# Kernel tuning notes

Measured on AMD Instinct MI355X. Metric: run time of the kernel, lower is better.

## Reference

```python
import jax, jax.numpy as jnp
import numpy as np

B, S, E, H, D = 4, 2048, 1024, 8, 128
EPS = 1e-5


def _ln(x, g, b):
    m = jnp.mean(x, axis=-1, keepdims=True)
    v = jnp.mean((x - m) ** 2, axis=-1, keepdims=True)
    return (x - m) * jax.lax.rsqrt(v + EPS) * g + b


def _xavier(k, shape, fan_in, fan_out):
    lim = float(np.sqrt(6.0 / (fan_in + fan_out)))
    return jax.random.uniform(k, shape, jnp.float32, -lim, lim)


def setup_inputs() -> dict:
    key = jax.random.key(0)
    ks = jax.random.split(key, 10)
    return {
        "x": jax.random.normal(ks[0], (B, S, E), jnp.float32),
        # embedding_to_z: Linear(E, H*D); stored as [E, H*D] for x @ W
        "W_ez": _xavier(ks[1], (E, H * D), E, H * D),
        "b_ez": jnp.zeros((H * D,), jnp.float32),
        "U_h": _xavier(ks[2], (H, D, D), D, D),
        "U_z": _xavier(ks[3], (H, D, D), D, D),
        "b_u": jnp.zeros((H, D), jnp.float32),
        "out_shaper": _xavier(ks[4], (H, D, D), D, D),
        # shared per-step state LayerNorm
        "lns_g": jnp.ones((D,), jnp.float32),
        "lns_b": jnp.zeros((D,), jnp.float32),
        # per-head FFN: LayerNorm(D) -> Linear(D,D) -> GELU -> Linear(D,E)
        "ff_ln_g": jnp.ones((H, D), jnp.float32),
        "ff_ln_b": jnp.zeros((H, D), jnp.float32),
        "ff_W1": _xavier(ks[5], (H, D, D), D, D),
        "ff_b1": jnp.zeros((H, D), jnp.float32),
        "ff_W2": _xavier(ks[6], (H, D, E), D, E),
        "ff_b2": jnp.zeros((H, E), jnp.float32),
        # layer_attention_weights: Linear(E, 1)
        "w_att": _xavier(ks[7], (E,), E, 1),
        "b_att": jnp.zeros((), jnp.float32),
        # output LayerNorm
        "lno_g": jnp.ones((E,), jnp.float32),
        "lno_b": jnp.zeros((E,), jnp.float32),
    }


def reference(x, W_ez, b_ez, U_h, U_z, b_u, out_shaper, lns_g, lns_b,
              ff_ln_g, ff_ln_b, ff_W1, ff_b1, ff_W2, ff_b2,
              w_att, b_att, lno_g, lno_b):
    b, s, _ = x.shape
    h, d = U_h.shape[0], U_h.shape[1]
    # z tokens: [B,S,H,D]
    z = jnp.tanh((x @ W_ez + b_ez).reshape(b, s, h, d))
    # torch.einsum('bhd,hdd->bhd') takes the DIAGONAL of the second operand
    uh_diag = jnp.einsum('hii->hi', U_h)          # [H,D]
    uz_diag = jnp.einsum('hii->hi', U_z)          # [H,D]
    os_diag = jnp.einsum('hii->hi', out_shaper)   # [H,D]

    def step(h_prev, z_t):
        # h_prev, z_t: [B,H,D]
        u = jax.nn.sigmoid(h_prev * uh_diag + z_t * uz_diag + b_u)
        h_new = u * h_prev + (1.0 - u) * z_t
        h_new = _ln(h_new, lns_g, lns_b)
        return h_new, h_new

    h0 = jnp.zeros((b, h, d), x.dtype)
    _, states = jax.lax.scan(step, h0, jnp.swapaxes(z, 0, 1))  # [S,B,H,D]
    states = jnp.swapaxes(states, 0, 1)                         # [B,S,H,D]

    shaped = states * os_diag                                   # diag einsum
    hln = _ln(shaped, ff_ln_g, ff_ln_b)                         # per-head LN
    h1 = jax.nn.gelu(jnp.einsum('bshd,hde->bshe', hln, ff_W1) + ff_b1,
                     approximate=False)                         # [B,S,H,D]
    ff_out = jnp.einsum('bshd,hde->bshe', h1, ff_W2) + ff_b2    # [B,S,H,E]

    scores = jax.nn.softmax(jnp.einsum('bshe,e->bsh', ff_out, w_att) + b_att,
                            axis=2)                             # over heads
    weighted = jnp.einsum('bshe,bsh->bse', ff_out, scores)      # [B,S,E]
    return _ln(weighted, lno_g, lno_b)
```

## Files before the change

kernel.cpp:

```cpp
#include <hip/hip_runtime.h>
#include <hip/hip_bf16.h>
#include <math.h>

#define BB 4
#define SS 2048
#define EE 1024
#define HH 8
#define DD 128
#define BSR (BB*SS)
#define HD  (HH*DD)
#define LNEPS 1e-5f
#define LOG2E 1.4426950408889634f

#define NCHUNK 16
#define CHS    128
#define TPC    64
#define NTICK  (NCHUNK*TPC)
#define NWORKER 256
#define SLOTF  (BB*CHS*1024)

#define FSCAN 16
#define FB    32
#define FD    96
#define FE    160

typedef __attribute__((ext_vector_type(8))) short bf16x8;
typedef __attribute__((ext_vector_type(4))) float f32x4;

__device__ __forceinline__ ushort f2bf(float f) {
    union { float f; unsigned u; } c{f};
    unsigned r = c.u + 0x7fff + ((c.u >> 16) & 1);
    return (ushort)(r >> 16);
}
__device__ __forceinline__ float bf2f(ushort b) {
    union { unsigned u; float f; } c{(unsigned)b << 16};
    return c.f;
}

typedef __attribute__((address_space(1))) const unsigned int GUI;
typedef __attribute__((address_space(3))) unsigned int LUI;
__device__ __forceinline__ void gl_lds16(const ushort* g, ushort* l) {
    __builtin_amdgcn_global_load_lds((GUI*)g, (LUI*)l, 16, 0, 0);
}

__device__ __forceinline__ float dpp_add(float x, const int ctrl) {
    int y;
    switch (ctrl) {
        case 0x111: y = __builtin_amdgcn_update_dpp(0, __float_as_int(x), 0x111, 0xf, 0xf, true); break;
        case 0x112: y = __builtin_amdgcn_update_dpp(0, __float_as_int(x), 0x112, 0xf, 0xf, true); break;
        case 0x114: y = __builtin_amdgcn_update_dpp(0, __float_as_int(x), 0x114, 0xf, 0xf, true); break;
        case 0x118: y = __builtin_amdgcn_update_dpp(0, __float_as_int(x), 0x118, 0xf, 0xf, true); break;
        case 0x142: y = __builtin_amdgcn_update_dpp(0, __float_as_int(x), 0x142, 0xf, 0xf, true); break;
        default:    y = __builtin_amdgcn_update_dpp(0, __float_as_int(x), 0x143, 0xf, 0xf, true); break;
    }
    return x + __int_as_float(y);
}

__device__ __forceinline__ float wave_sum64(float x) {
    x = dpp_add(x, 0x111);
    x = dpp_add(x, 0x112);
    x = dpp_add(x, 0x114);
    x = dpp_add(x, 0x118);
    x = dpp_add(x, 0x142);
    x = dpp_add(x, 0x143);
    return __int_as_float(__builtin_amdgcn_readlane(__float_as_int(x), 63));
}

__device__ __forceinline__ unsigned flag_peek(unsigned* f) {
    return __hip_atomic_fetch_add(f, 0u, __ATOMIC_RELAXED, __HIP_MEMORY_SCOPE_AGENT);
}
__device__ __forceinline__ void wait_ge(unsigned* f, unsigned tgt) {
    if (threadIdx.x == 0) {
        while (flag_peek(f) < tgt) __builtin_amdgcn_s_sleep(16);
        __builtin_amdgcn_fence(__ATOMIC_ACQUIRE, "agent");
    }
    __syncthreads();
}
__device__ __forceinline__ void done_inc(unsigned* f) {
    __syncthreads();
    if (threadIdx.x == 0) {
        __builtin_amdgcn_fence(__ATOMIC_RELEASE, "agent");
        __hip_atomic_fetch_add(f, 1u, __ATOMIC_RELAXED, __HIP_MEMORY_SCOPE_AGENT);
    }
}
__device__ __forceinline__ unsigned done_inc_ret(unsigned* f, unsigned* sh) {
    __syncthreads();
    if (threadIdx.x == 0) {
        __builtin_amdgcn_fence(__ATOMIC_RELEASE, "agent");
        *sh = __hip_atomic_fetch_add(f, 1u, __ATOMIC_RELAXED, __HIP_MEMORY_SCOPE_AGENT);
    }
    __syncthreads();
    return *sh;
}

__global__ __launch_bounds__(256)
void convx2_k(const float* __restrict__ x,
              ushort* __restrict__ hi, ushort* __restrict__ lo)
{
    const size_t idx = ((size_t)blockIdx.x * 256 + threadIdx.x) * 4;
    const float4 v = *(const float4*)(x + idx);
    ushort4 oh, ol;
    oh.x = f2bf(v.x); ol.x = f2bf(v.x - bf2f(oh.x));
    oh.y = f2bf(v.y); ol.y = f2bf(v.y - bf2f(oh.y));
    oh.z = f2bf(v.z); ol.z = f2bf(v.z - bf2f(oh.z));
    oh.w = f2bf(v.w); ol.w = f2bf(v.w - bf2f(oh.w));
    *(ushort4*)(hi + idx) = oh;
    *(ushort4*)(lo + idx) = ol;
}

__global__ __launch_bounds__(256)
void prepall_k(const float* __restrict__ W_ez,
               ushort* __restrict__ Wth, ushort* __restrict__ Wtl,
               const float* __restrict__ W2, ushort* __restrict__ W2t,
               const float* __restrict__ W1, ushort* __restrict__ W1t,
               const float* __restrict__ w_att, const float* __restrict__ b2,
               const float* __restrict__ b_att,
               const float* __restrict__ Uh, const float* __restrict__ Uz,
               const float* __restrict__ Os,
               float* __restrict__ q, float* __restrict__ c,
               float* __restrict__ uh_d, float* __restrict__ uz_d,
               float* __restrict__ os_d, unsigned* __restrict__ flags)
{
    __shared__ float tile[32][33];
    const int blk = blockIdx.x;
    if (blk == 2434) {
        flags[threadIdx.x] = 0;
        return;
    }
    const int tx = threadIdx.x & 31, ty = threadIdx.x >> 5;
    if (blk < 1024) {
        const int k0 = (blk >> 5) * 32, n0 = (blk & 31) * 32;
        #pragma unroll
        for (int i = 0; i < 4; ++i)
            tile[ty + i*8][tx] = W_ez[(size_t)(k0 + ty + i*8) * 1024 + n0 + tx];
        __syncthreads();
        #pragma unroll
        for (int i = 0; i < 4; ++i) {
            const float v = tile[tx][ty + i*8];
            const ushort h = f2bf(v);
            Wth[(size_t)(n0 + ty + i*8) * 1024 + k0 + tx] = h;
            Wtl[(size_t)(n0 + ty + i*8) * 1024 + k0 + tx] = f2bf(v - bf2f(h));
        }
    } else if (blk < 2048) {
        const int b2i = blk - 1024;
        const int k0 = (b2i >> 5) * 32, n0 = (b2i & 31) * 32;
        #pragma unroll
        for (int i = 0; i < 4; ++i)
            tile[ty + i*8][tx] = W2[(size_t)(k0 + ty + i*8) * 1024 + n0 + tx];
        __syncthreads();
        #pragma unroll
        for (int i = 0; i < 4; ++i)
            W2t[(size_t)(n0 + ty + i*8) * 1024 + k0 + tx] = f2bf(tile[tx][ty + i*8]);
    } else if (blk < 2176) {
        const int idx = blk - 2048;
        const int hh = idx >> 4;
        const int k0 = (idx & 3) * 32, n0 = ((idx >> 2) & 3) * 32;
        const float* Wb = W1 + (size_t)hh * DD * DD;
        ushort*      Wtb = W1t + (size_t)hh * DD * DD;
        #pragma unroll
        for (int i = 0; i < 4; ++i)
            tile[ty + i*8][tx] = Wb[(size_t)(k0 + ty + i*8) * DD + n0 + tx];
        __syncthreads();
        #pragma unroll
        for (int i = 0; i < 4; ++i)
            Wtb[(size_t)(n0 + ty + i*8) * DD + k0 + tx] = f2bf(tile[tx][ty + i*8]);
    } else {
        const int gid  = (blk - 2176) * 256 + threadIdx.x;
        const int wave = gid >> 6, lane = gid & 63;
        if (wave < HD) {
            const float* wp = W2 + (size_t)wave * EE;
            float p = 0.f;
            for (int e = lane; e < EE; e += 64) p = fmaf(wp[e], w_att[e], p);
            #pragma unroll
            for (int off = 32; off > 0; off >>= 1) p += __shfl_xor(p, off, 64);
            if (lane == 0) {
                q[wave] = p;
                const int h = wave >> 7, d = wave & 127;
                uh_d[wave] = Uh[(size_t)h*DD*DD + (size_t)d*DD + d];
                uz_d[wave] = Uz[(size_t)h*DD*DD + (size_t)d*DD + d];
                os_d[wave] = Os[(size_t)h*DD*DD + (size_t)d*DD + d];
            }
        } else if (wave < HD + HH) {
            const int h = wave - HD;
            const float* bp = b2 + (size_t)h * EE;
            float p = 0.f;
            for (int e = lane; e < EE; e += 64) p = fmaf(bp[e], w_att[e], p);
            #pragma unroll
            for (int off = 32; off > 0; off >>= 1) p += __shfl_xor(p, off, 64);
            if (lane == 0) c[h] = p + b_att[0];
        }
    }
}

__global__ __launch_bounds__(256)
void gemm_mfma_hp(const ushort* __restrict__ Ah, const ushort* __restrict__ Al,
                  const ushort* __restrict__ Bh, const ushort* __restrict__ Bl,
                  float* __restrict__ C, const float* __restrict__ bias)
{
    __shared__ ushort AsmH[128*32], AsmL[128*32];
    __shared__ ushort BsmH[128*32], BsmL[128*32];
    const int t = threadIdx.x, lane = t & 63, w = t >> 6;
    const int wr = w >> 1, wc = w & 1;
    const int row0 = blockIdx.x * 128, col0 = blockIdx.y * 128;

    const int lr = lane >> 2;
    const int lc = (lane & 3) ^ (lr & 3);
    const size_t aoff0 = (size_t)(row0 +      w*16 + lr) * 1024 + lc*8;
    const size_t aoff1 = (size_t)(row0 + 64 + w*16 + lr) * 1024 + lc*8;
    const size_t boff0 = (size_t)(col0 +      w*16 + lr) * 1024 + lc*8;
    const size_t boff1 = (size_t)(col0 + 64 + w*16 + lr) * 1024 + lc*8;
    ushort* AH0 = AsmH + (     w*16) * 32;  ushort* AH1 = AsmH + (64 + w*16) * 32;
    ushort* AL0 = AsmL + (     w*16) * 32;  ushort* AL1 = AsmL + (64 + w*16) * 32;
    ushort* BH0 = BsmH + (     w*16) * 32;  ushort* BH1 = BsmH + (64 + w*16) * 32;
    ushort* BL0 = BsmL + (     w*16) * 32;  ushort* BL1 = BsmL + (64 + w*16) * 32;

    f32x4 acc[4][4];
    #pragma unroll
    for (int i = 0; i < 4; ++i)
        #pragma unroll
        for (int j = 0; j < 4; ++j) acc[i][j] = (f32x4){0.f,0.f,0.f,0.f};

    const int quad = lane >> 4;
    const int fr   = lane & 15;
    const int fchk = (quad ^ (lane & 3)) * 8;

    for (int k0 = 0; k0 < 1024; k0 += 32) {
        __syncthreads();
        gl_lds16(Ah + aoff0 + k0, AH0);
        gl_lds16(Ah + aoff1 + k0, AH1);
        gl_lds16(Bh + boff0 + k0, BH0);
        gl_lds16(Bh + boff1 + k0, BH1);
        gl_lds16(Al + aoff0 + k0, AL0);
        gl_lds16(Al + aoff1 + k0, AL1);
        gl_lds16(Bl + boff0 + k0, BL0);
        gl_lds16(Bl + boff1 + k0, BL1);
        __syncthreads();

        bf16x8 afh[4], afl[4], bfh[4], bfl[4];
        #pragma unroll
        for (int i = 0; i < 4; ++i) {
            const int ra = (wr*64 + i*16 + fr) * 32 + fchk;
            afh[i] = *(const bf16x8*)(AsmH + ra);
            afl[i] = *(const bf16x8*)(AsmL + ra);
            const int rb = (wc*64 + i*16 + fr) * 32 + fchk;
            bfh[i] = *(const bf16x8*)(BsmH + rb);
            bfl[i] = *(const bf16x8*)(BsmL + rb);
        }
        #pragma unroll
        for (int i = 0; i < 4; ++i)
            #pragma unroll
            for (int j = 0; j < 4; ++j) {
                acc[i][j] = __builtin_amdgcn_mfma_f32_16x16x32_bf16(
                    afh[i], bfl[j], acc[i][j], 0, 0, 0);
                acc[i][j] = __builtin_amdgcn_mfma_f32_16x16x32_bf16(
                    afl[i], bfh[j], acc[i][j], 0, 0, 0);
                acc[i][j] = __builtin_amdgcn_mfma_f32_16x16x32_bf16(
                    afh[i], bfh[j], acc[i][j], 0, 0, 0);
            }
    }

    float colv[4];
    #pragma unroll
    for (int tj = 0; tj < 4; ++tj)
        colv[tj] = bias[col0 + wc*64 + tj*16 + fr];
    #pragma unroll
    for (int ti = 0; ti < 4; ++ti)
        #pragma unroll
        for (int i = 0; i < 4; ++i) {
            const int row = row0 + wr*64 + ti*16 + quad*4 + i;
            #pragma unroll
            for (int tj = 0; tj < 4; ++tj) {
                const int col = col0 + wc*64 + tj*16 + fr;
                C[(size_t)row*1024 + col] = tanhf(acc[ti][tj][i] + colv[tj]);
            }
        }
}

__global__ __launch_bounds__(256)
void pipeline_k(const float* __restrict__ z,
                const float* __restrict__ uh_d, const float* __restrict__ uz_d,
                const float* __restrict__ b_u,
                const float* __restrict__ lns_g, const float* __restrict__ lns_b,
                ushort* __restrict__ stb,
                const float* __restrict__ os_d,
                const float* __restrict__ ffg, const float* __restrict__ ffb,
                const ushort* __restrict__ W1t, const float* __restrict__ ff_b1,
                const float* __restrict__ qv, const float* __restrict__ cv,
                ushort* __restrict__ h1b, float* __restrict__ logits,
                const ushort* __restrict__ W2t, const float* __restrict__ ff_b2,
                float* __restrict__ wslots,
                const float* __restrict__ lno_g, const float* __restrict__ lno_b,
                float* __restrict__ out,
                unsigned* __restrict__ flags)
{
    if (blockIdx.x < 32) {
        if (threadIdx.x >= 64) return;
        const int bh = blockIdx.x;
        const int b = bh >> 3, h = bh & 7;
        const int l = threadIdx.x;
        const int d0 = 2*l, d1 = d0 + 1;

        const float uhn0 = -uh_d[h*DD+d0] * LOG2E, uhn1 = -uh_d[h*DD+d1] * LOG2E;
        const float uzn0 = -uz_d[h*DD+d0] * LOG2E, uzn1 = -uz_d[h*DD+d1] * LOG2E;
        const float bun0 = -b_u [h*DD+d0] * LOG2E, bun1 = -b_u [h*DD+d1] * LOG2E;
        const float g0  = lns_g[d0], g1 = lns_g[d1];
        const float be0 = lns_b[d0], be1 = lns_b[d1];
        const float A0 = g0 * uhn0, A1 = g1 * uhn1;
        const float bunB0 = fmaf(be0, uhn0, bun0);
        const float bunB1 = fmaf(be1, uhn1, bun1);

        const float* zp = z + ((size_t)b * SS * HH + h) * DD + d0;
        unsigned* op = (unsigned*)(stb + (size_t)b * SS * HD + h * DD) + l;

        const int CH = 8;
        float2 zc[CH], zn[CH];
        float pb0[CH], pb1[CH];
        #pragma unroll
        for (int i = 0; i < CH; ++i) zc[i] = *(const float2*)(zp + (size_t)i*HD);
        #pragma unroll
        for (int i = 0; i < CH; ++i) {
            pb0[i] = fmaf(zc[i].x, uzn0, bunB0);
            pb1[i] = fmaf(zc[i].y, uzn1, bunB1);
        }

        float r_c, wp0, wp1, W0, W1, dv0, dv1;

#define PACK_STORE(HP0, HP1, OFF) do {                                       \
            const unsigned pu0 = __float_as_uint(HP0) + 0x8000u;             \
            const unsigned pu1 = __float_as_uint(HP1) + 0x8000u;             \
            op[(size_t)(OFF) * (HD/2)] =                                     \
                __builtin_amdgcn_perm(pu1, pu0, 0x07060302u);                \
        } while (0)

#define SCAN_STEP(ZX, ZY, PB0v, PB1v, ZNX, ZNY, OFF) do {                    \
            const float t0 = fmaf(r_c, W0, (PB0v));                          \
            const float t1 = fmaf(r_c, W1, (PB1v));                          \
            const float e0 = __builtin_amdgcn_exp2f(t0);                     \
            const float e1 = __builtin_amdgcn_exp2f(t1);                     \
            const float u0 = __builtin_amdgcn_rcpf(1.f + e0);                \
            const float u1 = __builtin_amdgcn_rcpf(1.f + e1);                \
            const float hn0 = fmaf(u0, dv0, (ZX));                           \
            const float hn1 = fmaf(u1, dv1, (ZY));                           \
            const float s1 = wave_sum64(hn0 + hn1);                          \
            const float s2 = wave_sum64(fmaf(hn0, hn0, hn1*hn1));            \
            const float m   = s1 * (1.f/128.f);                              \
            const float var = fmaf(s2, 1.f/128.f, -m*m);                     \
            r_c = __builtin_amdgcn_rsqf(var + LNEPS);                        \
            wp0 = hn0 - m; wp1 = hn1 - m;                                    \
            W0 = wp0 * A0; W1 = wp1 * A1;                                    \
            const float hp0 = fmaf(wp0, r_c * g0, be0);                      \
            const float hp1 = fmaf(wp1, r_c * g1, be1);                      \
            PACK_STORE(hp0, hp1, OFF);                                       \
            dv0 = hp0 - (ZNX); dv1 = hp1 - (ZNY);                            \
        } while (0)

        {
            const float z0 = zc[0].x, z1 = zc[0].y;
            const float t0 = fmaf(z0, uzn0, bun0);
            const float t1 = fmaf(z1, uzn1, bun1);
            const float e0 = __builtin_amdgcn_exp2f(t0);
            const float e1 = __builtin_amdgcn_exp2f(t1);
            const float u0 = __builtin_amdgcn_rcpf(1.f + e0);
            const float u1 = __builtin_amdgcn_rcpf(1.f + e1);
            const float hn0 = fmaf(u0, -z0, z0);
            const float hn1 = fmaf(u1, -z1, z1);
            const float s1 = wave_sum64(hn0 + hn1);
            const float s2 = wave_sum64(fmaf(hn0, hn0, hn1*hn1));
            const float m   = s1 * (1.f/128.f);
            const float var = fmaf(s2, 1.f/128.f, -m*m);
            r_c = __builtin_amdgcn_rsqf(var + LNEPS);
            wp0 = hn0 - m; wp1 = hn1 - m;
            W0 = wp0 * A0; W1 = wp1 * A1;
            const float hp0 = fmaf(wp0, r_c * g0, be0);
            const float hp1 = fmaf(wp1, r_c * g1, be1);
            PACK_STORE(hp0, hp1, 0);
            dv0 = hp0 - zc[1].x; dv1 = hp1 - zc[1].y;
        }

        #pragma unroll
        for (int i = 0; i < CH; ++i)
            zn[i] = *(const float2*)(zp + (size_t)(CH+i)*HD);
        #pragma unroll
        for (int i = 1; i < CH; ++i) {
            const float znx = (i+1 < CH) ? zc[i+1].x : zn[0].x;
            const float zny = (i+1 < CH) ? zc[i+1].y : zn[0].y;
            SCAN_STEP(zc[i].x, zc[i].y, pb0[i], pb1[i], znx, zny, i);
        }
        #pragma unroll
        for (int i = 0; i < CH; ++i) {
            zc[i] = zn[i];
            pb0[i] = fmaf(zn[i].x, uzn0, bunB0);
            pb1[i] = fmaf(zn[i].y, uzn1, bunB1);
        }

        for (int s0 = CH; s0 < SS; s0 += CH) {
            if (s0 + CH < SS) {
                #pragma unroll
                for (int i = 0; i < CH; ++i)
                    zn[i] = *(const float2*)(zp + (size_t)(s0+CH+i)*HD);
            } else {
                #pragma unroll
                for (int i = 0; i < CH; ++i) zn[i] = make_float2(0.f, 0.f);
            }
            #pragma unroll
            for (int i = 0; i < CH; ++i) {
                const float znx = (i+1 < CH) ? zc[i+1].x : zn[0].x;
                const float zny = (i+1 < CH) ? zc[i+1].y : zn[0].y;
                SCAN_STEP(zc[i].x, zc[i].y, pb0[i], pb1[i], znx, zny, s0 + i);
            }
            #pragma unroll
            for (int i = 0; i < CH; ++i) {
                zc[i] = zn[i];
                pb0[i] = fmaf(zn[i].x, uzn0, bunB0);
                pb1[i] = fmaf(zn[i].y, uzn1, bunB1);
            }
            if ((s0 & (CHS-1)) == CHS - CH) {
                if (threadIdx.x == 0) {
                    __builtin_amdgcn_fence(__ATOMIC_RELEASE, "agent");
                    __hip_atomic_fetch_add(&flags[FSCAN + (s0 >> 7)], 1u,
                                           __ATOMIC_RELAXED, __HIP_MEMORY_SCOPE_AGENT);
                }
            }
        }
#undef SCAN_STEP
#undef PACK_STORE
        return;
    }

    __shared__ ushort ApS[4*128*32];
    __shared__ ushort Bsm[128*32];
    __shared__ float  sLDS[128][8];
    __shared__ float  lpart[128][2];
    __shared__ unsigned s_tk, s_old;
    const int tid = threadIdx.x;
    const int lane = tid & 63, w = tid >> 6;
    const int wr = w >> 1, wc = w & 1;
    const int lr = lane >> 2;
    const int lc = (lane & 3) ^ (lr & 3);
    const int quad = lane >> 4;
    const int fr   = lane & 15;
    const int fchk = (quad ^ (lane & 3)) * 8;

    for (;;) {
        __syncthreads();
        if (tid == 0) s_tk = __hip_atomic_fetch_add(&flags[0], 1u,
                               __ATOMIC_RELAXED, __HIP_MEMORY_SCOPE_AGENT);
        __syncthreads();
        const unsigned tk = s_tk;
        if (tk >= NTICK) return;
        const int c = (int)(tk / TPC);
        const int r = (int)(tk % TPC);

        if (r < 32) {
            wait_ge(&flags[FSCAN + c], 32);
            const int bb = r >> 3, hh = r & 7;
            const int row0 = bb*SS + c*CHS;

            {
                const int l = lane;
                const int d0 = 2*l, d1 = d0 + 1;
                const float osd0 = os_d[hh*DD + d0], osd1 = os_d[hh*DD + d1];
                const float fg0 = ffg[hh*DD + d0], fg1 = ffg[hh*DD + d1];
                const float fb0 = ffb[hh*DD + d0], fb1 = ffb[hh*DD + d1];
                const unsigned* st_u = (const unsigned*)stb;
                const int p  = l >> 4;
                const int j  = (l >> 2) & 3;
                unsigned* ApU = (unsigned*)ApS;
                for (int it = 0; it < 32; ++it) {
                    const int rloc = it*4 + w;
                    const unsigned v = st_u[(size_t)(row0 + rloc)*512 + hh*64 + l];
                    const float x0 = bf2f((ushort)(v & 0xffff)) * osd0;
                    const float x1 = bf2f((ushort)(v >> 16))    * osd1;
                    float s1 = x0 + x1;
                    float s2 = fmaf(x0, x0, x1*x1);
                    #pragma unroll
                    for (int off = 32; off > 0; off >>= 1) {
                        s1 += __shfl_xor(s1, off, 64);
                        s2 += __shfl_xor(s2, off, 64);
                    }
                    const float m   = s1 * (1.f/128.f);
                    const float var = fmaf(s2, 1.f/128.f, -m*m);
                    const float rr  = rsqrtf(var + LNEPS);
                    const float o0 = fmaf((x0 - m)*rr, fg0, fb0);
                    const float o1 = fmaf((x1 - m)*rr, fg1, fb1);
                    const unsigned pv = (unsigned)f2bf(o0) | ((unsigned)f2bf(o1) << 16);
                    const int js = j ^ (rloc & 3);
                    ApU[p*2048 + rloc*16 + js*4 + (l & 3)] = pv;
                }
            }
            __syncthreads();

            const ushort* Bg0 = W1t + (size_t)hh*DD*DD + (     w*16 + lr) * DD + lc*8;
            const ushort* Bg1 = W1t + (size_t)hh*DD*DD + (64 + w*16 + lr) * DD + lc*8;
            ushort* Bl0 = Bsm + (     w*16) * 32;
            ushort* Bl1 = Bsm + (64 + w*16) * 32;

            f32x4 acc[4][4];
            #pragma unroll
            for (int i = 0; i < 4; ++i)
                #pragma unroll
                for (int j2 = 0; j2 < 4; ++j2) acc[i][j2] = (f32x4){0.f,0.f,0.f,0.f};

            for (int k0 = 0; k0 < 128; k0 += 32) {
                __syncthreads();
                gl_lds16(Bg0 + k0, Bl0);
                gl_lds16(Bg1 + k0, Bl1);
                __syncthreads();

                const ushort* Ap = ApS + (k0 >> 5) * 4096;
                bf16x8 af[4], bf[4];
                #pragma unroll
                for (int i = 0; i < 4; ++i) {
                    af[i] = *(const bf16x8*)(Ap + (wr*64 + i*16 + fr)*32 + fchk);
                    bf[i] = *(const bf16x8*)(Bsm + (wc*64 + i*16 + fr)*32 + fchk);
                }
                #pragma unroll
                for (int i = 0; i < 4; ++i)
                    #pragma unroll
                    for (int j2 = 0; j2 < 4; ++j2)
                        acc[i][j2] = __builtin_amdgcn_mfma_f32_16x16x32_bf16(
                            af[i], bf[j2], acc[i][j2], 0, 0, 0);
            }

            float colv[4], qh[4];
            #pragma unroll
            for (int tj = 0; tj < 4; ++tj) {
                const int col = wc*64 + tj*16 + fr;
                colv[tj] = ff_b1[hh*DD + col];
                qh[tj]   = qv[hh*DD + col];
            }
            #pragma unroll
            for (int ti = 0; ti < 4; ++ti)
                #pragma unroll
                for (int i = 0; i < 4; ++i) {
                    const int row = row0 + wr*64 + ti*16 + quad*4 + i;
                    float p = 0.f;
                    #pragma unroll
                    for (int tj = 0; tj < 4; ++tj) {
                        const int col = wc*64 + tj*16 + fr;
                        float v = acc[ti][tj][i] + colv[tj];
                        v = 0.5f * v * (1.f + erff(v * 0.70710678118654752f));
                        h1b[(size_t)row*1024 + hh*DD + col] = f2bf(v);
                        p = fmaf(v, qh[tj], p);
                    }
                    p = dpp_add(p, 0x111);
                    p = dpp_add(p, 0x112);
                    p = dpp_add(p, 0x114);
                    p = dpp_add(p, 0x118);
                    if (fr == 15)
                        lpart[wr*64 + ti*16 + quad*4 + i][wc] = p;
                }
            __syncthreads();
            if (tid < 128)
                logits[(size_t)(row0 + tid)*HH + hh] = lpart[tid][0] + lpart[tid][1] + cv[hh];
            done_inc(&flags[FB + c*4 + bb]);
        } else {
            const int sub = r - 32;
            const int bb = sub >> 3, cb = sub & 7;
            wait_ge(&flags[FB + c*4 + bb], 8);
            if (c >= 8) wait_ge(&flags[FE + (c-8)*4 + bb], 1);
            const int row0 = bb*SS + c*CHS, col0 = cb*128;
            float* wslot = wslots + (size_t)(c & 7) * SLOTF;

            if (tid < 128) {
                const float4 l03 = *(const float4*)(logits + (size_t)(row0 + tid)*8);
                const float4 l47 = *(const float4*)(logits + (size_t)(row0 + tid)*8 + 4);
                float lv[8] = {l03.x,l03.y,l03.z,l03.w,l47.x,l47.y,l47.z,l47.w};
                float mx = -1e30f;
                #pragma unroll
                for (int i = 0; i < 8; ++i) mx = fmaxf(mx, lv[i]);
                float den = 0.f;
                #pragma unroll
                for (int i = 0; i < 8; ++i) den += __expf(lv[i] - mx);
                const float rden = 1.f / den;
                #pragma unroll
                for (int i = 0; i < 8; ++i) sLDS[tid][i] = __expf(lv[i] - mx) * rden;
            }
            __syncthreads();

            const ushort* Bg0 = W2t + (size_t)(col0 +      w*16 + lr) * 1024 + lc*8;
            const ushort* Bg1 = W2t + (size_t)(col0 + 64 + w*16 + lr) * 1024 + lc*8;
            ushort* Bl0 = Bsm + (     w*16) * 32;
            ushort* Bl1 = Bsm + (64 + w*16) * 32;
            const int rl0 = w*16 + lr, rl1 = 64 + w*16 + lr;

            f32x4 acc[4][4];
            #pragma unroll
            for (int i = 0; i < 4; ++i)
                #pragma unroll
                for (int j2 = 0; j2 < 4; ++j2) acc[i][j2] = (f32x4){0.f,0.f,0.f,0.f};

            for (int k0 = 0; k0 < 1024; k0 += 32) {
                __syncthreads();
                {
                    const int kk = k0 + lc*8;
                    const int hidx = kk >> 7;
                    bf16x8 a0 = *(const bf16x8*)(h1b + (size_t)(row0 + rl0)*1024 + kk);
                    bf16x8 a1 = *(const bf16x8*)(h1b + (size_t)(row0 + rl1)*1024 + kk);
                    const float sc0 = sLDS[rl0][hidx];
                    const float sc1 = sLDS[rl1][hidx];
                    bf16x8 w0, w1;
                    #pragma unroll
                    for (int e = 0; e < 8; ++e) {
                        w0[e] = (short)f2bf(bf2f((ushort)a0[e]) * sc0);
                        w1[e] = (short)f2bf(bf2f((ushort)a1[e]) * sc1);
                    }
                    *(bf16x8*)(ApS + (     w*16)*32 + lane*8) = w0;
                    *(bf16x8*)(ApS + (64 + w*16)*32 + lane*8) = w1;
                }
                gl_lds16(Bg0 + k0, Bl0);
                gl_lds16(Bg1 + k0, Bl1);
                __syncthreads();

                bf16x8 af[4], bf[4];
                #pragma unroll
                for (int i = 0; i < 4; ++i) {
                    af[i] = *(const bf16x8*)(ApS + (wr*64 + i*16 + fr)*32 + fchk);
                    bf[i] = *(const bf16x8*)(Bsm + (wc*64 + i*16 + fr)*32 + fchk);
                }
                #pragma unroll
                for (int i = 0; i < 4; ++i)
                    #pragma unroll
                    for (int j2 = 0; j2 < 4; ++j2)
                        acc[i][j2] = __builtin_amdgcn_mfma_f32_16x16x32_bf16(
                            af[i], bf[j2], acc[i][j2], 0, 0, 0);
            }

            float b2v[4][HH];
            #pragma unroll
            for (int tj = 0; tj < 4; ++tj) {
                const int col = col0 + wc*64 + tj*16 + fr;
                #pragma unroll
                for (int h = 0; h < HH; ++h) b2v[tj][h] = ff_b2[(size_t)h*EE + col];
            }
            #pragma unroll
            for (int ti = 0; ti < 4; ++ti)
                #pragma unroll
                for (int i = 0; i < 4; ++i) {
                    const int lrow = wr*64 + ti*16 + quad*4 + i;
                    float sc[HH];
                    #pragma unroll
                    for (int h = 0; h < HH; ++h) sc[h] = sLDS[lrow][h];
                    #pragma unroll
                    for (int tj = 0; tj < 4; ++tj) {
                        const int col = col0 + wc*64 + tj*16 + fr;
                        float bbv = 0.f;
                        #pragma unroll
                        for (int h = 0; h < HH; ++h) bbv = fmaf(sc[h], b2v[tj][h], bbv);
                        wslot[(size_t)(bb*128 + lrow)*1024 + col] = acc[ti][tj][i] + bbv;
                    }
                }

            const unsigned old = done_inc_ret(&flags[FD + c*4 + bb], &s_old);
            if (old == 7) {
                if (tid == 0) __builtin_amdgcn_fence(__ATOMIC_ACQUIRE, "agent");
                __syncthreads();
                const float* wsE = wslots + (size_t)(c & 7) * SLOTF
                                 + (size_t)bb * 128 * 1024;
                float4 gvq[4], bvq[4];
                #pragma unroll
                for (int q4 = 0; q4 < 4; ++q4) {
                    gvq[q4] = *(const float4*)(lno_g + lane*4 + q4*256);
                    bvq[q4] = *(const float4*)(lno_b + lane*4 + q4*256);
                }
                for (int it = 0; it < 32; ++it) {
                    const int rloc = it*4 + w;
                    const float* wp = wsE + (size_t)rloc*1024;
                    float4 vq[4];
                    float s1 = 0.f, s2 = 0.f;
                    #pragma unroll
                    for (int q4 = 0; q4 < 4; ++q4) {
                        vq[q4] = *(const float4*)(wp + lane*4 + q4*256);
                        s1 += vq[q4].x + vq[q4].y + vq[q4].z + vq[q4].w;
                        s2 += vq[q4].x*vq[q4].x + vq[q4].y*vq[q4].y
                            + vq[q4].z*vq[q4].z + vq[q4].w*vq[q4].w;
                    }
                    #pragma unroll
                    for (int off = 32; off > 0; off >>= 1) {
                        s1 += __shfl_xor(s1, off, 64);
                        s2 += __shfl_xor(s2, off, 64);
                    }
                    const float m   = s1 * (1.f/1024.f);
                    const float var = fmaf(s2, 1.f/1024.f, -m*m);
                    const float rr  = rsqrtf(var + LNEPS);
                    float* op = out + (size_t)(row0 + rloc)*1024;
                    #pragma unroll
                    for (int q4 = 0; q4 < 4; ++q4) {
                        float4 o;
                        o.x = fmaf((vq[q4].x - m)*rr, gvq[q4].x, bvq[q4].x);
                        o.y = fmaf((vq[q4].y - m)*rr, gvq[q4].y, bvq[q4].y);
                        o.z = fmaf((vq[q4].z - m)*rr, gvq[q4].z, bvq[q4].z);
                        o.w = fmaf((vq[q4].w - m)*rr, gvq[q4].w, bvq[q4].w);
                        *(float4*)(op + lane*4 + q4*256) = o;
                    }
                }
                done_inc(&flags[FE + c*4 + bb]);
            }
        }
    }
}

extern "C" void kernel_launch(void* const* d_in, const int* in_sizes, int n_in,
                              void* d_out, int out_size, void* d_ws, size_t ws_size,
                              hipStream_t stream)
{
    const float* x       = (const float*)d_in[0];
    const float* W_ez    = (const float*)d_in[1];
    const float* b_ez    = (const float*)d_in[2];
    const float* U_h     = (const float*)d_in[3];
    const float* U_z     = (const float*)d_in[4];
    const float* b_u     = (const float*)d_in[5];
    const float* outsh   = (const float*)d_in[6];
    const float* lns_g   = (const float*)d_in[7];
    const float* lns_b   = (const float*)d_in[8];
    const float* ff_ln_g = (const float*)d_in[9];
    const float* ff_ln_b = (const float*)d_in[10];
    const float* ff_W1   = (const float*)d_in[11];
    const float* ff_b1   = (const float*)d_in[12];
    const float* ff_W2   = (const float*)d_in[13];
    const float* ff_b2   = (const float*)d_in[14];
    const float* w_att   = (const float*)d_in[15];
    const float* b_att   = (const float*)d_in[16];
    const float* lno_g   = (const float*)d_in[17];
    const float* lno_b   = (const float*)d_in[18];
    float* out = (float*)d_out;

    float* ws = (float*)d_ws;
    const size_t NBIG = (size_t)BSR * HD;
    float* bufA = ws;
    float* bufB = ws + NBIG;
    float* bufC = ws + 2*NBIG;
    float* ext  = ws + 3*NBIG;
    ushort* W2t   = (ushort*)ext;
    ushort* W1t   = (ushort*)(ext + 512*1024);
    float* logits = ext + 512*1024 + 64*1024;
    float* qv     = logits + BSR*HH;
    float* cv     = qv + HD;
    float* uh_d   = cv + 8;
    float* uz_d   = uh_d + HD;
    float* os_d   = uz_d + HD;
    unsigned* flags = (unsigned*)(os_d + HD);
    ushort* xb_hi = (ushort*)bufB;
    ushort* xb_lo = (ushort*)bufB + NBIG;
    ushort* stb   = (ushort*)bufB;
    ushort* WezT_hi = (ushort*)bufC;
    ushort* WezT_lo = (ushort*)bufC + 1024*1024;
    ushort* h1b   = (ushort*)bufC;
    float*  wslots = bufC + 4*1024*1024;

    convx2_k<<<(BSR*EE/4)/256, 256, 0, stream>>>(x, xb_hi, xb_lo);
    prepall_k<<<2435, 256, 0, stream>>>(W_ez, WezT_hi, WezT_lo,
                                        ff_W2, W2t, ff_W1, W1t,
                                        w_att, ff_b2, b_att,
                                        U_h, U_z, outsh,
                                        qv, cv, uh_d, uz_d, os_d, flags);
    gemm_mfma_hp<<<dim3(64, 8), 256, 0, stream>>>(
        xb_hi, xb_lo, WezT_hi, WezT_lo, bufA, b_ez);
    pipeline_k<<<32 + NWORKER, 256, 0, stream>>>(
        bufA, uh_d, uz_d, b_u, lns_g, lns_b, stb,
        os_d, ff_ln_g, ff_ln_b,
        W1t, ff_b1, qv, cv, h1b, logits,
        W2t, ff_b2, wslots,
        lno_g, lno_b, out, flags);
}
```

Baseline: 601.9 us.

## Fuse input projection GEMM into persistent pipeline kernel with per-chunk flags

Removes the separate x@W_ez GEMM launch and instead runs its tiles as the first 512 work tickets of the persistent pipeline kernel, signalling per-chunk completion flags. The scan blocks now wait on those flags chunk by chunk, so the sequential recurrence can start as soon as its first chunk's z rows are ready instead of after the whole GEMM. The scan wave's priority is raised, workers drop to 224 and output slots to 6 to fit resources, and WezT buffers are relocated to avoid aliasing with h1b/wslots. This risks contention between the GEMM tiles and the latency-critical scan, and relies on the ticket order for progress.

```diff
diff --git a/kernel.cpp b/kernel.cpp
--- a/kernel.cpp
+++ b/kernel.cpp
@@ -14,15 +14,18 @@
 
 #define NCHUNK 16
 #define CHS    128
+#define NZT    512
 #define TPC    64
-#define NTICK  (NCHUNK*TPC)
-#define NWORKER 256
+#define NTICK  (NZT + NCHUNK*TPC)
+#define NWORKER 224
+#define NSLOT  6
 #define SLOTF  (BB*CHS*1024)
 
 #define FSCAN 16
 #define FB    32
 #define FD    96
 #define FE    160
+#define FZ    224
 
 typedef __attribute__((ext_vector_type(8))) short bf16x8;
 typedef __attribute__((ext_vector_type(4))) float f32x4;
@@ -75,6 +78,16 @@
         __builtin_amdgcn_fence(__ATOMIC_ACQUIRE, "agent");
     }
     __syncthreads();
+}
+__device__ __forceinline__ void wave_wait_ge(unsigned* f, unsigned tgt) {
+    unsigned v = 0;
+    for (;;) {
+        if (threadIdx.x == 0) v = flag_peek(f);
+        v = __shfl(v, 0, 64);
+        if (v >= tgt) break;
+        __builtin_amdgcn_s_sleep(8);
+    }
+    __builtin_amdgcn_fence(__ATOMIC_ACQUIRE, "agent");
 }
 __device__ __forceinline__ void done_inc(unsigned* f) {
     __syncthreads();
@@ -193,95 +206,14 @@
 }
 
 __global__ __launch_bounds__(256)
-void gemm_mfma_hp(const ushort* __restrict__ Ah, const ushort* __restrict__ Al,
-                  const ushort* __restrict__ Bh, const ushort* __restrict__ Bl,
-                  float* __restrict__ C, const float* __restrict__ bias)
-{
-    __shared__ ushort AsmH[128*32], AsmL[128*32];
-    __shared__ ushort BsmH[128*32], BsmL[128*32];
-    const int t = threadIdx.x, lane = t & 63, w = t >> 6;
-    const int wr = w >> 1, wc = w & 1;
-    const int row0 = blockIdx.x * 128, col0 = blockIdx.y * 128;
-
-    const int lr = lane >> 2;
-    const int lc = (lane & 3) ^ (lr & 3);
-    const size_t aoff0 = (size_t)(row0 +      w*16 + lr) * 1024 + lc*8;
-    const size_t aoff1 = (size_t)(row0 + 64 + w*16 + lr) * 1024 + lc*8;
-    const size_t boff0 = (size_t)(col0 +      w*16 + lr) * 1024 + lc*8;
-    const size_t boff1 = (size_t)(col0 + 64 + w*16 + lr) * 1024 + lc*8;
-    ushort* AH0 = AsmH + (     w*16) * 32;  ushort* AH1 = AsmH + (64 + w*16) * 32;
-    ushort* AL0 = AsmL + (     w*16) * 32;  ushort* AL1 = AsmL + (64 + w*16) * 32;
-    ushort* BH0 = BsmH + (     w*16) * 32;  ushort* BH1 = BsmH + (64 + w*16) * 32;
-    ushort* BL0 = BsmL + (     w*16) * 32;  ushort* BL1 = BsmL + (64 + w*16) * 32;
-
-    f32x4 acc[4][4];
-    #pragma unroll
-    for (int i = 0; i < 4; ++i)
-        #pragma unroll
-        for (int j = 0; j < 4; ++j) acc[i][j] = (f32x4){0.f,0.f,0.f,0.f};
-
-    const int quad = lane >> 4;
-    const int fr   = lane & 15;
-    const int fchk = (quad ^ (lane & 3)) * 8;
-
-    for (int k0 = 0; k0 < 1024; k0 += 32) {
-        __syncthreads();
-        gl_lds16(Ah + aoff0 + k0, AH0);
-        gl_lds16(Ah + aoff1 + k0, AH1);
-        gl_lds16(Bh + boff0 + k0, BH0);
-        gl_lds16(Bh + boff1 + k0, BH1);
-        gl_lds16(Al + aoff0 + k0, AL0);
-        gl_lds16(Al + aoff1 + k0, AL1);
-        gl_lds16(Bl + boff0 + k0, BL0);
-        gl_lds16(Bl + boff1 + k0, BL1);
-        __syncthreads();
-
-        bf16x8 afh[4], afl[4], bfh[4], bfl[4];
-        #pragma unroll
-        for (int i = 0; i < 4; ++i) {
-            const int ra = (wr*64 + i*16 + fr) * 32 + fchk;
-            afh[i] = *(const bf16x8*)(AsmH + ra);
-            afl[i] = *(const bf16x8*)(AsmL + ra);
-            const int rb = (wc*64 + i*16 + fr) * 32 + fchk;
-            bfh[i] = *(const bf16x8*)(BsmH + rb);
-            bfl[i] = *(const bf16x8*)(BsmL + rb);
-        }
-        #pragma unroll
-        for (int i = 0; i < 4; ++i)
-            #pragma unroll
-            for (int j = 0; j < 4; ++j) {
-                acc[i][j] = __builtin_amdgcn_mfma_f32_16x16x32_bf16(
-                    afh[i], bfl[j], acc[i][j], 0, 0, 0);
-                acc[i][j] = __builtin_amdgcn_mfma_f32_16x16x32_bf16(
-                    afl[i], bfh[j], acc[i][j], 0, 0, 0);
-                acc[i][j] = __builtin_amdgcn_mfma_f32_16x16x32_bf16(
-                    afh[i], bfh[j], acc[i][j], 0, 0, 0);
-            }
-    }
-
-    float colv[4];
-    #pragma unroll
-    for (int tj = 0; tj < 4; ++tj)
-        colv[tj] = bias[col0 + wc*64 + tj*16 + fr];
-    #pragma unroll
-    for (int ti = 0; ti < 4; ++ti)
-        #pragma unroll
-        for (int i = 0; i < 4; ++i) {
-            const int row = row0 + wr*64 + ti*16 + quad*4 + i;
-            #pragma unroll
-            for (int tj = 0; tj < 4; ++tj) {
-                const int col = col0 + wc*64 + tj*16 + fr;
-                C[(size_t)row*1024 + col] = tanhf(acc[ti][tj][i] + colv[tj]);
-            }
-        }
-}
-
-__global__ __launch_bounds__(256)
-void pipeline_k(const float* __restrict__ z,
+void pipeline_k(float* z,
+                const ushort* xbh, const ushort* xbl,
+                const ushort* __restrict__ Wzh, const ushort* __restrict__ Wzl,
+                const float* __restrict__ b_ez,
                 const float* __restrict__ uh_d, const float* __restrict__ uz_d,
                 const float* __restrict__ b_u,
                 const float* __restrict__ lns_g, const float* __restrict__ lns_b,
-                ushort* __restrict__ stb,
+                ushort* stb,
                 const float* __restrict__ os_d,
                 const float* __restrict__ ffg, const float* __restrict__ ffb,
                 const ushort* __restrict__ W1t, const float* __restrict__ ff_b1,
@@ -295,6 +227,7 @@
 {
     if (blockIdx.x < 32) {
         if (threadIdx.x >= 64) return;
+        __builtin_amdgcn_s_setprio(3);
         const int bh = blockIdx.x;
         const int b = bh >> 3, h = bh & 7;
         const int l = threadIdx.x;
@@ -311,6 +244,8 @@
 
         const float* zp = z + ((size_t)b * SS * HH + h) * DD + d0;
         unsigned* op = (unsigned*)(stb + (size_t)b * SS * HD + h * DD) + l;
+
+        wave_wait_ge(&flags[FZ + 0], 32);
 
         const int CH = 8;
         float2 zc[CH], zn[CH];
@@ -395,6 +330,8 @@
 
         for (int s0 = CH; s0 < SS; s0 += CH) {
             if (s0 + CH < SS) {
+                if (((s0 + CH) & (CHS-1)) == 0)
+                    wave_wait_ge(&flags[FZ + ((s0 + CH) >> 7)], 32);
                 #pragma unroll
                 for (int i = 0; i < CH; ++i)
                     zn[i] = *(const float2*)(zp + (size_t)(s0+CH+i)*HD);
@@ -448,8 +385,86 @@
         __syncthreads();
         const unsigned tk = s_tk;
         if (tk >= NTICK) return;
-        const int c = (int)(tk / TPC);
-        const int r = (int)(tk % TPC);
+
+        if (tk < NZT) {
+            const int zc = (int)(tk >> 5), zb = (int)((tk >> 3) & 3), zy = (int)(tk & 7);
+            const int row0 = zb*SS + zc*CHS, col0 = zy*128;
+            ushort* AH = ApS;
+            ushort* AL = ApS + 4096;
+            ushort* BH = ApS + 8192;
+            ushort* BL = ApS + 12288;
+            const size_t aoff0 = (size_t)(row0 +      w*16 + lr) * 1024 + lc*8;
+            const size_t aoff1 = (size_t)(row0 + 64 + w*16 + lr) * 1024 + lc*8;
+            const size_t boff0 = (size_t)(col0 +      w*16 + lr) * 1024 + lc*8;
+            const size_t boff1 = (size_t)(col0 + 64 + w*16 + lr) * 1024 + lc*8;
+            ushort* AH0 = AH + (     w*16) * 32;  ushort* AH1 = AH + (64 + w*16) * 32;
+            ushort* AL0 = AL + (     w*16) * 32;  ushort* AL1 = AL + (64 + w*16) * 32;
+            ushort* BH0 = BH + (     w*16) * 32;  ushort* BH1 = BH + (64 + w*16) * 32;
+            ushort* BL0 = BL + (     w*16) * 32;  ushort* BL1 = BL + (64 + w*16) * 32;
+
+            f32x4 acc[4][4];
+            #pragma unroll
+            for (int i = 0; i < 4; ++i)
+                #pragma unroll
+                for (int j = 0; j < 4; ++j) acc[i][j] = (f32x4){0.f,0.f,0.f,0.f};
+
+            for (int k0 = 0; k0 < 1024; k0 += 32) {
+                __syncthreads();
+                gl_lds16(xbh + aoff0 + k0, AH0);
+                gl_lds16(xbh + aoff1 + k0, AH1);
+                gl_lds16(Wzh + boff0 + k0, BH0);
+                gl_lds16(Wzh + boff1 + k0, BH1);
+                gl_lds16(xbl + aoff0 + k0, AL0);
+                gl_lds16(xbl + aoff1 + k0, AL1);
+                gl_lds16(Wzl + boff0 + k0, BL0);
+                gl_lds16(Wzl + boff1 + k0, BL1);
+                __syncthreads();
+
+                bf16x8 afh[4], afl[4], bfh[4], bfl[4];
+                #pragma unroll
+                for (int i = 0; i < 4; ++i) {
+                    const int ra = (wr*64 + i*16 + fr) * 32 + fchk;
+                    afh[i] = *(const bf16x8*)(AH + ra);
+                    afl[i] = *(const bf16x8*)(AL + ra);
+                    const int rb = (wc*64 + i*16 + fr) * 32 + fchk;
+                    bfh[i] = *(const bf16x8*)(BH + rb);
+                    bfl[i] = *(const bf16x8*)(BL + rb);
+                }
+                #pragma unroll
+                for (int i = 0; i < 4; ++i)
+                    #pragma unroll
+                    for (int j = 0; j < 4; ++j) {
+                        acc[i][j] = __builtin_amdgcn_mfma_f32_16x16x32_bf16(
+                            afh[i], bfl[j], acc[i][j], 0, 0, 0);
+                        acc[i][j] = __builtin_amdgcn_mfma_f32_16x16x32_bf16(
+                            afl[i], bfh[j], acc[i][j], 0, 0, 0);
+                        acc[i][j] = __builtin_amdgcn_mfma_f32_16x16x32_bf16(
+                            afh[i], bfh[j], acc[i][j], 0, 0, 0);
+                    }
+            }
+
+            float colv[4];
+            #pragma unroll
+            for (int tj = 0; tj < 4; ++tj)
+                colv[tj] = b_ez[col0 + wc*64 + tj*16 + fr];
+            #pragma unroll
+            for (int ti = 0; ti < 4; ++ti)
+                #pragma unroll
+                for (int i = 0; i < 4; ++i) {
+                    const int row = row0 + wr*64 + ti*16 + quad*4 + i;
+                    #pragma unroll
+                    for (int tj = 0; tj < 4; ++tj) {
+                        const int col = col0 + wc*64 + tj*16 + fr;
+                        z[(size_t)row*1024 + col] = tanhf(acc[ti][tj][i] + colv[tj]);
+                    }
+                }
+            done_inc(&flags[FZ + zc]);
+            continue;
+        }
+
+        const unsigned t2 = tk - NZT;
+        const int c = (int)(t2 / TPC);
+        const int r = (int)(t2 % TPC);
 
         if (r < 32) {
             wait_ge(&flags[FSCAN + c], 32);
@@ -558,9 +573,9 @@
             const int sub = r - 32;
             const int bb = sub >> 3, cb = sub & 7;
             wait_ge(&flags[FB + c*4 + bb], 8);
-            if (c >= 8) wait_ge(&flags[FE + (c-8)*4 + bb], 1);
+            if (c >= NSLOT) wait_ge(&flags[FE + (c-NSLOT)*4 + bb], 1);
             const int row0 = bb*SS + c*CHS, col0 = cb*128;
-            float* wslot = wslots + (size_t)(c & 7) * SLOTF;
+            float* wslot = wslots + (size_t)(c % NSLOT) * SLOTF;
 
             if (tid < 128) {
                 const float4 l03 = *(const float4*)(logits + (size_t)(row0 + tid)*8);
@@ -655,7 +670,7 @@
             if (old == 7) {
                 if (tid == 0) __builtin_amdgcn_fence(__ATOMIC_ACQUIRE, "agent");
                 __syncthreads();
-                const float* wsE = wslots + (size_t)(c & 7) * SLOTF
+                const float* wsE = wslots + (size_t)(c % NSLOT) * SLOTF
                                  + (size_t)bb * 128 * 1024;
                 float4 gvq[4], bvq[4];
                 #pragma unroll
@@ -743,10 +758,10 @@
     ushort* xb_hi = (ushort*)bufB;
     ushort* xb_lo = (ushort*)bufB + NBIG;
     ushort* stb   = (ushort*)bufB;
-    ushort* WezT_hi = (ushort*)bufC;
-    ushort* WezT_lo = (ushort*)bufC + 1024*1024;
-    ushort* h1b   = (ushort*)bufC;
-    float*  wslots = bufC + 4*1024*1024;
+    ushort* h1b     = (ushort*)bufC;
+    float*  wslots  = bufC + 4*1024*1024;
+    ushort* WezT_hi = (ushort*)(bufC + 7*1024*1024);
+    ushort* WezT_lo = WezT_hi + 1024*1024;
 
     convx2_k<<<(BSR*EE/4)/256, 256, 0, stream>>>(x, xb_hi, xb_lo);
     prepall_k<<<2435, 256, 0, stream>>>(W_ez, WezT_hi, WezT_lo,
@@ -754,10 +769,9 @@
                                         w_att, ff_b2, b_att,
                                         U_h, U_z, outsh,
                                         qv, cv, uh_d, uz_d, os_d, flags);
-    gemm_mfma_hp<<<dim3(64, 8), 256, 0, stream>>>(
-        xb_hi, xb_lo, WezT_hi, WezT_lo, bufA, b_ez);
     pipeline_k<<<32 + NWORKER, 256, 0, stream>>>(
-        bufA, uh_d, uz_d, b_u, lns_g, lns_b, stb,
+        bufA, xb_hi, xb_lo, WezT_hi, WezT_lo, b_ez,
+        uh_d, uz_d, b_u, lns_g, lns_b, stb,
         os_d, ff_ln_g, ff_ln_b,
         W1t, ff_b1, qv, cv, h1b, logits,
         W2t, ff_b2, wslots,
```

New measurement: 616.7 us. 2.5% more time.
